# Kernel optimization log

Hardware: AMD Instinct MI355X
Metric: run time of the kernel (lower is better)

Reference implementation:

```python
import jax, jax.numpy as jnp
import numpy as np

NEUMANN_TERMS = 6  # matches neumann_terms=6 in init_kwargs


def cayley_apply(W, x, terms):
    """Apply Cayley-parameterized unitary U = (I - A)^{-1}(I + A), A = skew(W),
    with the inverse approximated by a truncated Neumann series:
    (I - A)^{-1} z ~= sum_{k=0}^{terms-1} A^k z.  x: [N, d] row vectors."""
    A = 0.5 * (W - W.T)            # skew-symmetric [d, d]
    z = x + x @ A.T                # (I + A) x
    acc = z
    s = z
    for _ in range(terms - 1):     # small fixed loop over Neumann terms
        s = s @ A.T                # A^k z
        acc = acc + s
    return acc


def quantum_activation(h, theta):
    """Parametric quantum rotation: rotate each adjacent feature pair by theta.
    Norm-preserving (unitary) nonlinearity in place of ReLU/GELU."""
    a = h[..., 0::2]
    b = h[..., 1::2]
    c = jnp.cos(theta)
    s = jnp.sin(theta)
    ra = a * c - b * s
    rb = a * s + b * c
    return jnp.stack([ra, rb], axis=-1).reshape(h.shape)


def setup_inputs() -> dict:
    key = jax.random.key(0)
    k1, k2, k3 = jax.random.split(key, 3)
    num_tokens, d_model = 16384, 2048
    x = jax.random.normal(k1, (num_tokens, d_model), dtype=jnp.float32)
    # Orthogonal(gain=0.1)-like init: small-norm weights keep the Neumann series convergent
    u1 = 0.1 * jax.random.normal(k2, (d_model, d_model), dtype=jnp.float32) / jnp.sqrt(d_model)
    u1 = u1 * jnp.sqrt(d_model) * 0.0 + 0.1 * jax.random.orthogonal(k2, d_model, dtype=jnp.float32)
    u2 = 0.1 * jax.random.orthogonal(k3, d_model, dtype=jnp.float32)
    theta = jnp.asarray(0.7854, dtype=jnp.float32)  # pi/4 initializer
    return {"x": x, "u1": u1, "u2": u2, "theta": theta}


def reference(x, u1, u2, theta):
    h = cayley_apply(u1, x, NEUMANN_TERMS)
    h = quantum_activation(h, theta)
    out = cayley_apply(u2, h, NEUMANN_TERMS)
    return out
```

## Files before the change

kernel.cpp:

```cpp
#include <hip/hip_runtime.h>
#include <hip/hip_bf16.h>

#define ND 2048

using bf16 = __hip_bfloat16;
using short8 = __attribute__((ext_vector_type(8))) short;
using floatx4 = __attribute__((ext_vector_type(4))) float;

__device__ __forceinline__ void gl2lds16(const short* g, short* l) {
    __builtin_amdgcn_global_load_lds(
        (const __attribute__((address_space(1))) unsigned int*)g,
        (__attribute__((address_space(3))) unsigned int*)l,
        16, 0, 0);
}

__device__ __forceinline__ int xcd_swz(int b, int g) {
    if ((g & 7) == 0) b = (b & 7) * (g >> 3) + (b >> 3);
    return b;
}


__global__ void build_skew2(const float* __restrict__ uA, bf16* __restrict__ MA,
                            const float* __restrict__ uB, bf16* __restrict__ MB) {
    __shared__ float t[32][33];
    const int nb = (ND / 32) * (ND / 32);
    int b = blockIdx.x;
    const float* u = uA;
    bf16* M = MA;
    if (b >= nb) { b -= nb; u = uB; M = MB; }
    const int bx = b & (ND / 32 - 1);
    const int by = b / (ND / 32);
    const int tx = threadIdx.x & 31;
    const int ty = threadIdx.x >> 5;
#pragma unroll
    for (int rr = 0; rr < 4; ++rr) {
        const int r = ty * 4 + rr;
        t[tx][r] = u[(size_t)(bx * 32 + r) * ND + by * 32 + tx];
    }
    __syncthreads();
#pragma unroll
    for (int rr = 0; rr < 4; ++rr) {
        const int r = ty * 4 + rr;
        const size_t idx = (size_t)(by * 32 + r) * ND + bx * 32 + tx;
        M[idx] = __float2bfloat16(0.5f * (t[r][tx] - u[idx]));
    }
}

__global__ void build_hoffs(const bf16* M2, const bf16* Q2, bf16* H2, bf16* HT2,
                            const bf16* M1, const bf16* Q1, bf16* H1) {
    const size_t nper = (size_t)ND * ND / 8;
    size_t g = (size_t)blockIdx.x * 256 + threadIdx.x;
    const bool second = (g >= nper);
    if (second) g -= nper;
    const size_t i8 = g * 8;
    const short8 mv = *(const short8*)((const short*)(second ? M1 : M2) + i8);
    const short8 qv = *(const short8*)((const short*)(second ? Q1 : Q2) + i8);
    short8 h, ht;
#pragma unroll
    for (int j = 0; j < 8; ++j) {
        const float m = __bfloat162float(__builtin_bit_cast(bf16, (short)mv[j]));
        const float q = __bfloat162float(__builtin_bit_cast(bf16, (short)qv[j]));
        h[j]  = __builtin_bit_cast(short, __float2bfloat16(2.f * m + q));
        ht[j] = __builtin_bit_cast(short, __float2bfloat16(q - 2.f * m));
    }
    if (second) {
        *(short8*)((short*)H1 + i8) = h;
    } else {
        *(short8*)((short*)H2 + i8) = h;
        *(short8*)((short*)HT2 + i8) = ht;
    }
}

__global__ void build_hoff(const bf16* M, const bf16* Msq, bf16* Hoff, bf16* HoffT) {
    const size_t idx = (size_t)blockIdx.x * 256 + threadIdx.x;
    const float m = __bfloat162float(M[idx]);
    const float q = __bfloat162float(Msq[idx]);
    Hoff[idx] = __float2bfloat16(2.f * m + q);
    HoffT[idx] = __float2bfloat16(q - 2.f * m);
}

__global__ void convert_f32_bf16(const float* __restrict__ x, bf16* __restrict__ y) {
    const size_t base = ((size_t)blockIdx.x * 256 + threadIdx.x) * 8;
    const float4 f0 = *(const float4*)(x + base);
    const float4 f1 = *(const float4*)(x + base + 4);
    short8 pk;
    pk[0] = __builtin_bit_cast(short, __float2bfloat16(f0.x));
    pk[1] = __builtin_bit_cast(short, __float2bfloat16(f0.y));
    pk[2] = __builtin_bit_cast(short, __float2bfloat16(f0.z));
    pk[3] = __builtin_bit_cast(short, __float2bfloat16(f0.w));
    pk[4] = __builtin_bit_cast(short, __float2bfloat16(f1.x));
    pk[5] = __builtin_bit_cast(short, __float2bfloat16(f1.y));
    pk[6] = __builtin_bit_cast(short, __float2bfloat16(f1.z));
    pk[7] = __builtin_bit_cast(short, __float2bfloat16(f1.w));
    *(short8*)((short*)y + base) = pk;
}

enum { EPI_PLAIN = 0, EPI_NEG = 1, EPI_ADD1 = 2, EPI_P = 3, EPI_P_ROT = 4 };

template <int EPI, bool OF32>
__device__ __forceinline__ void gemm_core(
    short* aT, short* bT,
    const bf16* __restrict__ A, const bf16* __restrict__ Bt, void* __restrict__ Cp,
    const int Nc, const int K, const int bx, const int by,
    const bf16* __restrict__ add1, const bf16* __restrict__ add2,
    const float* __restrict__ thetaP)
{
    const int tid = threadIdx.x;
    const int lane = tid & 63;
    const int quad = lane >> 4;
    const int l15 = lane & 15;
    const int wv = tid >> 6;
    const int wr = (wv >> 1) << 6;
    const int wc = (wv & 1) << 6;

    const short* Ag = (const short*)A + (size_t)(by << 7) * K;
    const short* Bg = (const short*)Bt + (size_t)(bx << 7) * K;

    floatx4 acc[4][4];
#pragma unroll
    for (int i = 0; i < 4; ++i)
#pragma unroll
        for (int j = 0; j < 4; ++j)
            acc[i][j] = (floatx4){0.f, 0.f, 0.f, 0.f};

    for (int k0 = 0; k0 < K; k0 += 32) {
#pragma unroll
        for (int c = 0; c < 2; ++c) {
            const int ch = (c << 8) + (wv << 6) + lane;
            const int row = ch >> 2;
            const int kp = (ch & 3) << 3;
            const int ldsBase = ((c << 8) + (wv << 6)) << 3;
            gl2lds16(Ag + (size_t)row * K + k0 + kp, aT + ldsBase);
            gl2lds16(Bg + (size_t)row * K + k0 + kp, bT + ldsBase);
        }
        __syncthreads();
        short8 af[4], bfr[4];
#pragma unroll
        for (int mi = 0; mi < 4; ++mi)
            af[mi] = *(const short8*)(aT + ((wr + (mi << 4) + l15) << 5) + (quad << 3));
#pragma unroll
        for (int ni = 0; ni < 4; ++ni)
            bfr[ni] = *(const short8*)(bT + ((wc + (ni << 4) + l15) << 5) + (quad << 3));
#pragma unroll
        for (int mi = 0; mi < 4; ++mi)
#pragma unroll
            for (int ni = 0; ni < 4; ++ni)
                acc[mi][ni] = __builtin_amdgcn_mfma_f32_16x16x32_bf16(af[mi], bfr[ni], acc[mi][ni], 0, 0, 0);
        __syncthreads();
    }

    float ct = 0.f, st = 0.f;
    if (EPI == EPI_P_ROT) {
        const float th = *thetaP;
        ct = cosf(th);
        st = sinf(th);
    }

#pragma unroll
    for (int mi = 0; mi < 4; ++mi) {
#pragma unroll
        for (int ni = 0; ni < 4; ++ni) {
#pragma unroll
            for (int r = 0; r < 4; ++r) {
                const int row = (by << 7) + wr + (mi << 4) + (quad << 2) + r;
                const int col = (bx << 7) + wc + (ni << 4) + l15;
                const size_t idx = (size_t)row * Nc + col;
                float v = acc[mi][ni][r];
                if (EPI == EPI_NEG) v = -v;
                if (EPI == EPI_ADD1) v += __bfloat162float(add1[idx]);
                if (EPI == EPI_P)
                    v += (row == col ? 1.f : 0.f)
                       + __bfloat162float(add1[idx]) + __bfloat162float(add2[idx]);
                if (EPI == EPI_P_ROT) {
                    v += (row == col ? 1.f : 0.f)
                       + __bfloat162float(add1[idx]) + __bfloat162float(add2[idx]);
                    const float w = __shfl_xor(v, 1, 64);
                    v = (l15 & 1) ? (st * w + ct * v) : (ct * v - st * w);
                }
                if (OF32) ((float*)Cp)[idx] = v;
                else      ((bf16*)Cp)[idx] = __float2bfloat16(v);
            }
        }
    }
}

template <int EPI, bool OF32>
__launch_bounds__(256, 2) __global__
void gemm_one(const bf16* __restrict__ A, const bf16* __restrict__ Bt,
              void* __restrict__ Cp, const int Nc, const int K,
              const bf16* __restrict__ add1, const bf16* __restrict__ add2,
              const float* __restrict__ thetaP)
{
    __shared__ __attribute__((aligned(16))) short aT[128 * 32];
    __shared__ __attribute__((aligned(16))) short bT[128 * 32];
    const int nblk = Nc >> 7;
    const int b = xcd_swz(blockIdx.x, gridDim.x);
    gemm_core<EPI, OF32>(aT, bT, A, Bt, Cp, Nc, K, b % nblk, b / nblk,
                         add1, add2, thetaP);
}

template <int EPI0, int EPI1>
__launch_bounds__(256, 2) __global__
void gemm_dual(const bf16* A0, const bf16* B0, bf16* C0, const bf16* a10, const bf16* a20,
               const bf16* A1, const bf16* B1, bf16* C1, const bf16* a11, const bf16* a21,
               const float* thetaP)
{
    __shared__ __attribute__((aligned(16))) short aT[128 * 32];
    __shared__ __attribute__((aligned(16))) short bT[128 * 32];
    const int nblk = ND >> 7;
    const int nsub = nblk * nblk;
    int b = xcd_swz(blockIdx.x, gridDim.x);
    if (b < nsub) {
        gemm_core<EPI0, false>(aT, bT, A0, B0, (void*)C0, ND, ND, b % nblk, b / nblk, a10, a20, thetaP);
    } else {
        b -= nsub;
        gemm_core<EPI1, false>(aT, bT, A1, B1, (void*)C1, ND, ND, b % nblk, b / nblk, a11, a21, thetaP);
    }
}


__device__ __forceinline__ void stage512(short* ldsT, const short* gT, const int K,
                                         const int kb, const int c0,
                                         const int wv, const int lane) {
    const int ch = c0 + (wv << 6) + lane;
    const int rw = ch >> 3;
    const int cs = (ch & 7) ^ (rw & 7);
    gl2lds16(gT + (size_t)rw * K + kb + (cs << 3),
             ldsT + ((c0 + (wv << 6)) << 3));
}

__device__ __forceinline__ void phase_mid() {
    __builtin_amdgcn_sched_barrier(0);
    __builtin_amdgcn_s_barrier();
    asm volatile("s_waitcnt lgkmcnt(0)" ::: "memory");
    __builtin_amdgcn_sched_barrier(0);
    __builtin_amdgcn_s_setprio(1);
}
__device__ __forceinline__ void phase_end() {
    __builtin_amdgcn_s_setprio(0);
    __builtin_amdgcn_sched_barrier(0);
    __builtin_amdgcn_s_barrier();
}

#define MFMA_BF16 __builtin_amdgcn_mfma_f32_16x16x32_bf16

__device__ __forceinline__ void tile256(
    short* Ac, short* Bc, short* An,
    const short* Ag, const short* Bg, const int K, const int nt, const int t,
    const int wv, const int lane, const int aBase, const int bBase,
    const int cOff0, const int cOff1, floatx4 (&acc)[8][4])
{
    short8 af[4][2], bb[4][2];
    const int kb1 = (t + 1) << 6;
    const int kb2 = (t + 2) << 6;

#pragma unroll
    for (int ml = 0; ml < 4; ++ml) {
        af[ml][0] = *(const short8*)(Ac + aBase + (ml << 10) + cOff0);
        af[ml][1] = *(const short8*)(Ac + aBase + (ml << 10) + cOff1);
    }
#pragma unroll
    for (int ni = 0; ni < 2; ++ni) {
        bb[ni][0] = *(const short8*)(Bc + bBase + (ni << 10) + cOff0);
        bb[ni][1] = *(const short8*)(Bc + bBase + (ni << 10) + cOff1);
    }
    if (t + 1 < nt) { stage512(An, Ag, K, kb1, 512, wv, lane); stage512(An, Ag, K, kb1, 1536, wv, lane); }
    __builtin_amdgcn_sched_barrier(0);
    asm volatile("s_waitcnt lgkmcnt(8)" ::: "memory");
    phase_mid();
#pragma unroll
    for (int ml = 0; ml < 4; ++ml)
#pragma unroll
        for (int ni = 0; ni < 2; ++ni) {
            acc[ml][ni] = MFMA_BF16(af[ml][0], bb[ni][0], acc[ml][ni], 0, 0, 0);
            acc[ml][ni] = MFMA_BF16(af[ml][1], bb[ni][1], acc[ml][ni], 0, 0, 0);
        }
    phase_end();

#pragma unroll
    for (int ni = 2; ni < 4; ++ni) {
        bb[ni][0] = *(const short8*)(Bc + bBase + (ni << 10) + cOff0);
        bb[ni][1] = *(const short8*)(Bc + bBase + (ni << 10) + cOff1);
    }
    if (t + 2 < nt) { stage512(Ac, Ag, K, kb2, 0, wv, lane); stage512(Ac, Ag, K, kb2, 1024, wv, lane); }
    phase_mid();
#pragma unroll
    for (int ml = 0; ml < 4; ++ml)
#pragma unroll
        for (int ni = 2; ni < 4; ++ni) {
            acc[ml][ni] = MFMA_BF16(af[ml][0], bb[ni][0], acc[ml][ni], 0, 0, 0);
            acc[ml][ni] = MFMA_BF16(af[ml][1], bb[ni][1], acc[ml][ni], 0, 0, 0);
        }
    phase_end();

#pragma unroll
    for (int ml = 0; ml < 4; ++ml) {
        af[ml][0] = *(const short8*)(Ac + aBase + 4096 + (ml << 10) + cOff0);
        af[ml][1] = *(const short8*)(Ac + aBase + 4096 + (ml << 10) + cOff1);
    }
    if (t + 2 < nt) { stage512(Bc, Bg, K, kb2, 0, wv, lane); stage512(Bc, Bg, K, kb2, 512, wv, lane); }
    phase_mid();
#pragma unroll
    for (int ml = 0; ml < 4; ++ml)
#pragma unroll
        for (int ni = 0; ni < 2; ++ni) {
            acc[4 + ml][ni] = MFMA_BF16(af[ml][0], bb[ni][0], acc[4 + ml][ni], 0, 0, 0);
            acc[4 + ml][ni] = MFMA_BF16(af[ml][1], bb[ni][1], acc[4 + ml][ni], 0, 0, 0);
        }
    phase_end();

    if (t + 2 < nt) { stage512(Bc, Bg, K, kb2, 1024, wv, lane); stage512(Bc, Bg, K, kb2, 1536, wv, lane); }
    __builtin_amdgcn_sched_barrier(0);
    if (t < nt - 2) asm volatile("s_waitcnt vmcnt(6)" ::: "memory");
    else            asm volatile("s_waitcnt vmcnt(0)" ::: "memory");
    __builtin_amdgcn_s_barrier();
    __builtin_amdgcn_sched_barrier(0);
    __builtin_amdgcn_s_setprio(1);
#pragma unroll
    for (int ml = 0; ml < 4; ++ml)
#pragma unroll
        for (int ni = 2; ni < 4; ++ni) {
            acc[4 + ml][ni] = MFMA_BF16(af[ml][0], bb[ni][0], acc[4 + ml][ni], 0, 0, 0);
            acc[4 + ml][ni] = MFMA_BF16(af[ml][1], bb[ni][1], acc[4 + ml][ni], 0, 0, 0);
        }
    phase_end();
}

__launch_bounds__(512, 2) __global__
void gemm_big256(const bf16* __restrict__ A, const bf16* __restrict__ Bt,
                 float* __restrict__ C, const int Nc, const int K)
{
    __shared__ __attribute__((aligned(16))) short smem[65536];
    short* A0s = smem;
    short* A1s = smem + 16384;
    short* B0s = smem + 32768;
    short* B1s = smem + 49152;

    const int nblkx = Nc >> 8;
    const int b = xcd_swz(blockIdx.x, gridDim.x);
    const int bx = b % nblkx;
    const int by = b / nblkx;
    const int tid = threadIdx.x;
    const int lane = tid & 63;
    const int q = lane >> 4;
    const int l15 = lane & 15;
    const int wv = tid >> 6;
    const int wm = wv >> 2;
    const int wn = wv & 3;

    const short* Ag = (const short*)A + (size_t)(by << 8) * K;
    const short* Bg = (const short*)Bt + (size_t)(bx << 8) * K;

    const int swz = l15 & 7;
    const int aBase = ((wm << 7) + l15) << 6;
    const int bBase = ((wn << 6) + l15) << 6;
    const int cOff0 = (q ^ swz) << 3;
    const int cOff1 = ((q + 4) ^ swz) << 3;

    floatx4 acc[8][4];
#pragma unroll
    for (int i = 0; i < 8; ++i)
#pragma unroll
        for (int j = 0; j < 4; ++j)
            acc[i][j] = (floatx4){0.f, 0.f, 0.f, 0.f};

    const int nt = K >> 6;

    stage512(A0s, Ag, K, 0, 0,    wv, lane);
    stage512(A0s, Ag, K, 0, 512,  wv, lane);
    stage512(A0s, Ag, K, 0, 1024, wv, lane);
    stage512(A0s, Ag, K, 0, 1536, wv, lane);
    stage512(B0s, Bg, K, 0, 0,    wv, lane);
    stage512(B0s, Bg, K, 0, 512,  wv, lane);
    stage512(B0s, Bg, K, 0, 1024, wv, lane);
    stage512(B0s, Bg, K, 0, 1536, wv, lane);
    stage512(A1s, Ag, K, 64, 0,    wv, lane);
    stage512(A1s, Ag, K, 64, 1024, wv, lane);
    stage512(B1s, Bg, K, 64, 0,    wv, lane);
    stage512(B1s, Bg, K, 64, 512,  wv, lane);
    stage512(B1s, Bg, K, 64, 1024, wv, lane);
    stage512(B1s, Bg, K, 64, 1536, wv, lane);
    __builtin_amdgcn_sched_barrier(0);
    asm volatile("s_waitcnt vmcnt(6)" ::: "memory");
    __builtin_amdgcn_s_barrier();

    for (int t = 0; t < nt; t += 2) {
        tile256(A0s, B0s, A1s, Ag, Bg, K, nt, t,     wv, lane, aBase, bBase, cOff0, cOff1, acc);
        tile256(A1s, B1s, A0s, Ag, Bg, K, nt, t + 1, wv, lane, aBase, bBase, cOff0, cOff1, acc);
    }

#pragma unroll
    for (int mi = 0; mi < 8; ++mi)
#pragma unroll
        for (int ni = 0; ni < 4; ++ni)
#pragma unroll
            for (int r = 0; r < 4; ++r) {
                const int row = (by << 8) + (wm << 7) + (mi << 4) + (q << 2) + r;
                const int col = (bx << 8) + (wn << 6) + (ni << 4) + l15;
                C[(size_t)row * Nc + col] = acc[mi][ni][r];
            }
}

template <int EPI, bool AF32, bool OF32>
__launch_bounds__(256, 2) __global__
void gemm_bt(const void* __restrict__ Ap, const bf16* __restrict__ Bt,
             void* __restrict__ Cp, const int Nc, const int K,
             const bf16* __restrict__ add1, const bf16* __restrict__ add2,
             const float* __restrict__ thetaP)
{
    __shared__ __attribute__((aligned(16))) short aT[128 * 32];
    __shared__ __attribute__((aligned(16))) short bT[128 * 32];

    const int nblk = Nc >> 7;
    const int bx = blockIdx.x % nblk;
    const int by = blockIdx.x / nblk;
    const int tid = threadIdx.x;
    const int lane = tid & 63;
    const int quad = lane >> 4;
    const int l15 = lane & 15;
    const int wv = tid >> 6;
    const int wr = (wv >> 1) << 6;
    const int wc = (wv & 1) << 6;

    const short* Ag = (const short*)Ap + (size_t)(by << 7) * K;
    const float* Agf = (const float*)Ap + (size_t)(by << 7) * K;
    const short* Bg = (const short*)Bt + (size_t)(bx << 7) * K;

    floatx4 acc[4][4];
#pragma unroll
    for (int i = 0; i < 4; ++i)
#pragma unroll
        for (int j = 0; j < 4; ++j)
            acc[i][j] = (floatx4){0.f, 0.f, 0.f, 0.f};

    for (int k0 = 0; k0 < K; k0 += 32) {
#pragma unroll
        for (int c = 0; c < 2; ++c) {
            const int ch = tid + (c << 8);
            const int row = ch >> 2;
            const int kp = (ch & 3) << 3;
            if (AF32) {
                const float4 f0 = *(const float4*)(Agf + (size_t)row * K + k0 + kp);
                const float4 f1 = *(const float4*)(Agf + (size_t)row * K + k0 + kp + 4);
                short8 pk;
                pk[0] = __builtin_bit_cast(short, __float2bfloat16(f0.x));
                pk[1] = __builtin_bit_cast(short, __float2bfloat16(f0.y));
                pk[2] = __builtin_bit_cast(short, __float2bfloat16(f0.z));
                pk[3] = __builtin_bit_cast(short, __float2bfloat16(f0.w));
                pk[4] = __builtin_bit_cast(short, __float2bfloat16(f1.x));
                pk[5] = __builtin_bit_cast(short, __float2bfloat16(f1.y));
                pk[6] = __builtin_bit_cast(short, __float2bfloat16(f1.z));
                pk[7] = __builtin_bit_cast(short, __float2bfloat16(f1.w));
                *(short8*)(aT + (row << 5) + kp) = pk;
            } else {
                *(int4*)(aT + (row << 5) + kp) = *(const int4*)(Ag + (size_t)row * K + k0 + kp);
            }
            *(int4*)(bT + (row << 5) + kp) = *(const int4*)(Bg + (size_t)row * K + k0 + kp);
        }
        __syncthreads();
        short8 af[4], bfr[4];
#pragma unroll
        for (int mi = 0; mi < 4; ++mi)
            af[mi] = *(const short8*)(aT + ((wr + (mi << 4) + l15) << 5) + (quad << 3));
#pragma unroll
        for (int ni = 0; ni < 4; ++ni)
            bfr[ni] = *(const short8*)(bT + ((wc + (ni << 4) + l15) << 5) + (quad << 3));
#pragma unroll
        for (int mi = 0; mi < 4; ++mi)
#pragma unroll
            for (int ni = 0; ni < 4; ++ni)
                acc[mi][ni] = __builtin_amdgcn_mfma_f32_16x16x32_bf16(af[mi], bfr[ni], acc[mi][ni], 0, 0, 0);
        __syncthreads();
    }

    float ct = 0.f, st = 0.f;
    if (EPI == EPI_P_ROT) {
        const float th = *thetaP;
        ct = cosf(th);
        st = sinf(th);
    }

#pragma unroll
    for (int mi = 0; mi < 4; ++mi) {
#pragma unroll
        for (int ni = 0; ni < 4; ++ni) {
#pragma unroll
            for (int r = 0; r < 4; ++r) {
                const int row = (by << 7) + wr + (mi << 4) + (quad << 2) + r;
                const int col = (bx << 7) + wc + (ni << 4) + l15;
                const size_t idx = (size_t)row * Nc + col;
                float v = acc[mi][ni][r];
                if (EPI == EPI_NEG) v = -v;
                if (EPI == EPI_ADD1) v += __bfloat162float(add1[idx]);
                if (EPI == EPI_P || EPI == EPI_P_ROT)
                    v += (row == col ? 1.f : 0.f)
                       + __bfloat162float(add1[idx]) + __bfloat162float(add2[idx]);
                if (EPI == EPI_P_ROT) {
                    const float w = __shfl_xor(v, 1, 64);
                    v = (l15 & 1) ? (st * w + ct * v) : (ct * v - st * w);
                }
                if (OF32) ((float*)Cp)[idx] = v;
                else      ((bf16*)Cp)[idx] = __float2bfloat16(v);
            }
        }
    }
}


extern "C" void kernel_launch(void* const* d_in, const int* in_sizes, int n_in,
                              void* d_out, int out_size, void* d_ws, size_t ws_size,
                              hipStream_t stream)
{
    const float* x = (const float*)d_in[0];
    const float* u1 = (const float*)d_in[1];
    const float* u2 = (const float*)d_in[2];
    const float* th = (const float*)d_in[3];
    float* out = (float*)d_out;
    const int tokens = in_sizes[0] / ND;

    const size_t MAT = (size_t)ND * ND;
    const size_t XBE = (size_t)tokens * ND;

    const dim3 blk(256);
    const int gSkew = (ND / 32) * (ND / 32);
    const int gElem = (int)(MAT / 256);
    const int gSm = (ND / 128) * (ND / 128);
    const int gBig = (tokens / 128) * (ND / 128);

    if (ws_size >= (6 * MAT + XBE) * sizeof(bf16)) {
        bf16* base = (bf16*)d_ws;
        bf16* b0 = base;
        bf16* b1 = base + MAT;
        bf16* b2 = base + 2 * MAT;
        bf16* b3 = base + 3 * MAT;
        bf16* b4 = base + 4 * MAT;
        bf16* b5 = base + 5 * MAT;
        bf16* xb = base + 6 * MAT;

        convert_f32_bf16<<<(int)(XBE / 2048), blk, 0, stream>>>(x, xb);
        build_skew2<<<2 * gSkew, blk, 0, stream>>>(u2, b0, u1, b1);
        gemm_dual<EPI_NEG, EPI_NEG><<<2 * gSm, blk, 0, stream>>>(
            b0, b0, b2, nullptr, nullptr,  b1, b1, b3, nullptr, nullptr, nullptr);
        gemm_dual<EPI_ADD1, EPI_ADD1><<<2 * gSm, blk, 0, stream>>>(
            b2, b2, b4, b2, nullptr,  b3, b3, b5, b3, nullptr, nullptr);
        build_hoffs<<<(int)(2 * MAT / 2048), blk, 0, stream>>>(b0, b2, b2, b0, b1, b3, b3);
        gemm_dual<EPI_P, EPI_P_ROT><<<2 * gSm, blk, 0, stream>>>(
            b4, b2, b0, b4, b0,  b3, b5, b1, b5, b3, th);
        gemm_one<EPI_PLAIN, false><<<gSm, blk, 0, stream>>>(b0, b1, b2, ND, ND, nullptr, nullptr, nullptr);
        if ((tokens & 255) == 0) {
            const int gBig256 = (tokens >> 8) * (ND >> 8);
            gemm_big256<<<gBig256, dim3(512), 0, stream>>>(xb, b2, out, ND, ND);
        } else {
            gemm_one<EPI_PLAIN, true><<<gBig, blk, 0, stream>>>(xb, b2, out, ND, ND, nullptr, nullptr, nullptr);
        }
    } else {
        bf16* A = (bf16*)d_ws;
        bf16* B = A + MAT;
        bf16* Cb = B + MAT;
        bf16* D = Cb + MAT;
        bf16* E = D + MAT;

        build_skew2<<<gSkew, blk, 0, stream>>>(u2, A, u2, A);
        gemm_bt<EPI_NEG, false, false><<<gSm, blk, 0, stream>>>(A, A, B, ND, ND, nullptr, nullptr, nullptr);
        gemm_bt<EPI_ADD1, false, false><<<gSm, blk, 0, stream>>>(B, B, Cb, ND, ND, B, nullptr, nullptr);
        build_hoff<<<gElem, blk, 0, stream>>>(A, B, D, E);
        gemm_bt<EPI_P, false, false><<<gSm, blk, 0, stream>>>(Cb, D, A, ND, ND, Cb, E, nullptr);

        build_skew2<<<gSkew, blk, 0, stream>>>(u1, B, u1, B);
        gemm_bt<EPI_NEG, false, false><<<gSm, blk, 0, stream>>>(B, B, Cb, ND, ND, nullptr, nullptr, nullptr);
        gemm_bt<EPI_ADD1, false, false><<<gSm, blk, 0, stream>>>(Cb, Cb, D, ND, ND, Cb, nullptr, nullptr);
        build_hoff<<<gElem, blk, 0, stream>>>(B, Cb, E, B);
        gemm_bt<EPI_P_ROT, false, false><<<gSm, blk, 0, stream>>>(E, D, Cb, ND, ND, D, E, th);

        gemm_bt<EPI_PLAIN, false, false><<<gSm, blk, 0, stream>>>(A, Cb, D, ND, ND, nullptr, nullptr, nullptr);
        gemm_bt<EPI_PLAIN, true, true><<<gBig, blk, 0, stream>>>(x, D, out, ND, ND, nullptr, nullptr, nullptr);
    }
}
```

Baseline: 563.9 us.

## Split-K the 2048x2048 weight-composition GEMMs with fp32 partials and reduce kernels

Replaces the dual 128-tile GEMMs that build the composite weight matrices with a split-K 256-tile GEMM (gemm_sk), which writes fp32 partial sums into the output buffer used as scratch. Separate elementwise reduce kernels then sum the partials and apply the epilogues (negate, add, identity, theta rotation). The aim is to fill the GPU better, since a 2048x2048 GEMM with 256 tiles gives only 64 blocks, and to reuse the faster 256-tile pipeline. In exchange it adds extra fp32 traffic and more kernel launches, and the scratch reuse depends on the output buffer being large enough.

Measured after the change: 593.6 us. 5.3% more time.

```diff
diff --git a/kernel.cpp b/kernel.cpp
--- a/kernel.cpp
+++ b/kernel.cpp
@@ -93,6 +93,122 @@
     pk[6] = __builtin_bit_cast(short, __float2bfloat16(f1.z));
     pk[7] = __builtin_bit_cast(short, __float2bfloat16(f1.w));
     *(short8*)((short*)y + base) = pk;
+}
+
+__device__ __forceinline__ void loadS8(const float* p, float (&v)[8]) {
+    const float4 a = *(const float4*)p;
+    const float4 b = *(const float4*)(p + 4);
+    v[0] = a.x; v[1] = a.y; v[2] = a.z; v[3] = a.w;
+    v[4] = b.x; v[5] = b.y; v[6] = b.z; v[7] = b.w;
+}
+#define BF(x)   __bfloat162float(__builtin_bit_cast(bf16, (short)(x)))
+#define TOBF(x) __builtin_bit_cast(short, __float2bfloat16(x))
+
+__global__ void red_msq_hoff(const float* __restrict__ S,
+                             bf16* M2io ,
+                             bf16* M1io ,
+                             bf16* Msq2o , bf16* Msq1o ,
+                             bf16* Hoff2o ) {
+    const size_t MATE = (size_t)ND * ND;
+    const size_t nper = MATE / 8;
+    size_t g = (size_t)blockIdx.x * 256 + threadIdx.x;
+    const bool c1 = (g >= nper);
+    if (c1) g -= nper;
+    const size_t i8 = g * 8;
+    const float* s0 = S + (c1 ? 2 * MATE : 0) + i8;
+    float p0[8], p1[8];
+    loadS8(s0, p0); loadS8(s0 + MATE, p1);
+    const short8 mv = *(const short8*)((const short*)(c1 ? M1io : M2io) + i8);
+    short8 msq, hf, ht;
+#pragma unroll
+    for (int j = 0; j < 8; ++j) {
+        const short qb = TOBF(-(p0[j] + p1[j]));
+        msq[j] = qb;
+        const float q = BF(qb);
+        const float m = BF(mv[j]);
+        hf[j] = TOBF(2.f * m + q);
+        ht[j] = TOBF(q - 2.f * m);
+    }
+    if (c1) {
+        *(short8*)((short*)Msq1o + i8) = msq;
+        *(short8*)((short*)M1io + i8) = hf;
+    } else {
+        *(short8*)((short*)Msq2o + i8) = msq;
+        *(short8*)((short*)Hoff2o + i8) = hf;
+        *(short8*)((short*)M2io + i8) = ht;
+    }
+}
+
+__global__ void red_goff(const float* __restrict__ S, bf16* g2io , bf16* g1io ) {
+    const size_t MATE = (size_t)ND * ND;
+    const size_t nper = MATE / 8;
+    size_t g = (size_t)blockIdx.x * 256 + threadIdx.x;
+    const bool c1 = (g >= nper);
+    if (c1) g -= nper;
+    const size_t i8 = g * 8;
+    const float* s0 = S + (c1 ? 2 * MATE : 0) + i8;
+    float p0[8], p1[8];
+    loadS8(s0, p0); loadS8(s0 + MATE, p1);
+    const short8 av = *(const short8*)((const short*)(c1 ? g1io : g2io) + i8);
+    short8 o;
+#pragma unroll
+    for (int j = 0; j < 8; ++j)
+        o[j] = TOBF((p0[j] + p1[j]) + BF(av[j]));
+    *(short8*)((short*)(c1 ? g1io : g2io) + i8) = o;
+}
+
+__global__ void red_p(const float* __restrict__ S,
+                      bf16* p2t , const bf16* goff2 ,
+                      bf16* p1r , const bf16* goff1 ,
+                      const float* __restrict__ thetaP) {
+    const size_t MATE = (size_t)ND * ND;
+    const size_t nper = MATE / 8;
+    size_t g = (size_t)blockIdx.x * 256 + threadIdx.x;
+    const bool c1 = (g >= nper);
+    if (c1) g -= nper;
+    const size_t i8 = g * 8;
+    const float* s0 = S + (c1 ? 2 * MATE : 0) + i8;
+    float p0[8], p1[8];
+    loadS8(s0, p0); loadS8(s0 + MATE, p1);
+    const short8 a1v = *(const short8*)((const short*)(c1 ? goff1 : goff2) + i8);
+    const short8 a2v = *(const short8*)((const short*)(c1 ? p1r : p2t) + i8);
+    float v[8];
+#pragma unroll
+    for (int j = 0; j < 8; ++j) {
+        const size_t e = i8 + j;
+        const float diag = ((e >> 11) == (e & (ND - 1))) ? 1.f : 0.f;
+        v[j] = p0[j] + p1[j];
+        v[j] += diag + BF(a1v[j]) + BF(a2v[j]);
+    }
+    short8 o;
+    if (c1) {
+        const float th = *thetaP;
+        const float ct = cosf(th), st = sinf(th);
+#pragma unroll
+        for (int j = 0; j < 8; j += 2) {
+            const float a = v[j], b = v[j + 1];
+            o[j]     = TOBF(ct * a - st * b);
+            o[j + 1] = TOBF(st * a + ct * b);
+        }
+        *(short8*)((short*)p1r + i8) = o;
+    } else {
+#pragma unroll
+        for (int j = 0; j < 8; ++j) o[j] = TOBF(v[j]);
+        *(short8*)((short*)p2t + i8) = o;
+    }
+}
+
+__global__ void red_qt(const float* __restrict__ S, bf16* __restrict__ q) {
+    const size_t MATE = (size_t)ND * ND;
+    const size_t i8 = ((size_t)blockIdx.x * 256 + threadIdx.x) * 8;
+    float p0[8], p1[8], p2[8], p3[8];
+    loadS8(S + i8, p0); loadS8(S + MATE + i8, p1);
+    loadS8(S + 2 * MATE + i8, p2); loadS8(S + 3 * MATE + i8, p3);
+    short8 o;
+#pragma unroll
+    for (int j = 0; j < 8; ++j)
+        o[j] = TOBF(((p0[j] + p1[j]) + p2[j]) + p3[j]);
+    *(short8*)((short*)q + i8) = o;
 }
 
 enum { EPI_PLAIN = 0, EPI_NEG = 1, EPI_ADD1 = 2, EPI_P = 3, EPI_P_ROT = 4 };
@@ -247,12 +363,13 @@
 __device__ __forceinline__ void tile256(
     short* Ac, short* Bc, short* An,
     const short* Ag, const short* Bg, const int K, const int nt, const int t,
+    const int kOff,
     const int wv, const int lane, const int aBase, const int bBase,
     const int cOff0, const int cOff1, floatx4 (&acc)[8][4])
 {
     short8 af[4][2], bb[4][2];
-    const int kb1 = (t + 1) << 6;
-    const int kb2 = (t + 2) << 6;
+    const int kb1 = kOff + ((t + 1) << 6);
+    const int kb2 = kOff + ((t + 2) << 6);
 
 #pragma unroll
     for (int ml = 0; ml < 4; ++ml) {
@@ -385,8 +502,8 @@
     __builtin_amdgcn_s_barrier();
 
     for (int t = 0; t < nt; t += 2) {
-        tile256(A0s, B0s, A1s, Ag, Bg, K, nt, t,     wv, lane, aBase, bBase, cOff0, cOff1, acc);
-        tile256(A1s, B1s, A0s, Ag, Bg, K, nt, t + 1, wv, lane, aBase, bBase, cOff0, cOff1, acc);
+        tile256(A0s, B0s, A1s, Ag, Bg, K, nt, t,     0, wv, lane, aBase, bBase, cOff0, cOff1, acc);
+        tile256(A1s, B1s, A0s, Ag, Bg, K, nt, t + 1, 0, wv, lane, aBase, bBase, cOff0, cOff1, acc);
     }
 
 #pragma unroll
@@ -398,6 +515,88 @@
                 const int row = (by << 8) + (wm << 7) + (mi << 4) + (q << 2) + r;
                 const int col = (bx << 8) + (wn << 6) + (ni << 4) + l15;
                 C[(size_t)row * Nc + col] = acc[mi][ni][r];
+            }
+}
+
+template <int NT>
+__launch_bounds__(512, 2) __global__
+void gemm_sk(const bf16* __restrict__ A0, const bf16* __restrict__ B0,
+             const bf16* __restrict__ A1, const bf16* __restrict__ B1,
+             float* __restrict__ S)
+{
+    __shared__ __attribute__((aligned(16))) short smem[65536];
+    short* A0s = smem;
+    short* A1s = smem + 16384;
+    short* B0s = smem + 32768;
+    short* B1s = smem + 49152;
+
+    const int b = xcd_swz(blockIdx.x, gridDim.x);
+    const int sub = b >> 6;
+    const int t6 = b & 63;
+    const int bx = t6 & 7;
+    const int by = t6 >> 3;
+    const bf16* A; const bf16* Bt; int kOff;
+    if (NT == 16) { A = (sub & 2) ? A1 : A0; Bt = (sub & 2) ? B1 : B0; kOff = (sub & 1) << 10; }
+    else          { A = A0; Bt = B0; kOff = sub << 9; }
+    float* C = S + (size_t)sub * ((size_t)ND * ND);
+    const int K = ND;
+
+    const int tid = threadIdx.x;
+    const int lane = tid & 63;
+    const int q = lane >> 4;
+    const int l15 = lane & 15;
+    const int wv = tid >> 6;
+    const int wm = wv >> 2;
+    const int wn = wv & 3;
+
+    const short* Ag = (const short*)A + (size_t)(by << 8) * K;
+    const short* Bg = (const short*)Bt + (size_t)(bx << 8) * K;
+
+    const int swz = l15 & 7;
+    const int aBase = ((wm << 7) + l15) << 6;
+    const int bBase = ((wn << 6) + l15) << 6;
+    const int cOff0 = (q ^ swz) << 3;
+    const int cOff1 = ((q + 4) ^ swz) << 3;
+
+    floatx4 acc[8][4];
+#pragma unroll
+    for (int i = 0; i < 8; ++i)
+#pragma unroll
+        for (int j = 0; j < 4; ++j)
+            acc[i][j] = (floatx4){0.f, 0.f, 0.f, 0.f};
+
+    stage512(A0s, Ag, K, kOff, 0,    wv, lane);
+    stage512(A0s, Ag, K, kOff, 512,  wv, lane);
+    stage512(A0s, Ag, K, kOff, 1024, wv, lane);
+    stage512(A0s, Ag, K, kOff, 1536, wv, lane);
+    stage512(B0s, Bg, K, kOff, 0,    wv, lane);
+    stage512(B0s, Bg, K, kOff, 512,  wv, lane);
+    stage512(B0s, Bg, K, kOff, 1024, wv, lane);
+    stage512(B0s, Bg, K, kOff, 1536, wv, lane);
+    stage512(A1s, Ag, K, kOff + 64, 0,    wv, lane);
+    stage512(A1s, Ag, K, kOff + 64, 1024, wv, lane);
+    stage512(B1s, Bg, K, kOff + 64, 0,    wv, lane);
+    stage512(B1s, Bg, K, kOff + 64, 512,  wv, lane);
+    stage512(B1s, Bg, K, kOff + 64, 1024, wv, lane);
+    stage512(B1s, Bg, K, kOff + 64, 1536, wv, lane);
+    __builtin_amdgcn_sched_barrier(0);
+    asm volatile("s_waitcnt vmcnt(6)" ::: "memory");
+    __builtin_amdgcn_s_barrier();
+
+    for (int t = 0; t < NT; t += 2) {
+        tile256(A0s, B0s, A1s, Ag, Bg, K, NT, t,     kOff, wv, lane, aBase, bBase, cOff0, cOff1, acc);
+        tile256(A1s, B1s, A0s, Ag, Bg, K, NT, t + 1, kOff, wv, lane, aBase, bBase, cOff0, cOff1, acc);
+    }
+
+#pragma unroll
+    for (int mi = 0; mi < 8; ++mi)
+#pragma unroll
+        for (int ni = 0; ni < 4; ++ni)
+#pragma unroll
+            for (int r = 0; r < 4; ++r) {
+                const int row = (by << 8) + (wm << 7) + (mi << 4) + (q << 2) + r;
+                const int col = (bx << 8) + (wn << 6) + (ni << 4) + l15;
+                C[(size_t)row * ND + col] = acc[mi][ni][r];
             }
 }
 
@@ -534,23 +733,34 @@
         bf16* b2 = base + 2 * MAT;
         bf16* b3 = base + 3 * MAT;
         bf16* b4 = base + 4 * MAT;
-        bf16* b5 = base + 5 * MAT;
         bf16* xb = base + 6 * MAT;
 
         convert_f32_bf16<<<(int)(XBE / 2048), blk, 0, stream>>>(x, xb);
         build_skew2<<<2 * gSkew, blk, 0, stream>>>(u2, b0, u1, b1);
-        gemm_dual<EPI_NEG, EPI_NEG><<<2 * gSm, blk, 0, stream>>>(
-            b0, b0, b2, nullptr, nullptr,  b1, b1, b3, nullptr, nullptr, nullptr);
-        gemm_dual<EPI_ADD1, EPI_ADD1><<<2 * gSm, blk, 0, stream>>>(
-            b2, b2, b4, b2, nullptr,  b3, b3, b5, b3, nullptr, nullptr);
-        build_hoffs<<<(int)(2 * MAT / 2048), blk, 0, stream>>>(b0, b2, b2, b0, b1, b3, b3);
-        gemm_dual<EPI_P, EPI_P_ROT><<<2 * gSm, blk, 0, stream>>>(
-            b4, b2, b0, b4, b0,  b3, b5, b1, b5, b3, th);
-        gemm_one<EPI_PLAIN, false><<<gSm, blk, 0, stream>>>(b0, b1, b2, ND, ND, nullptr, nullptr, nullptr);
-        if ((tokens & 255) == 0) {
+
+        if ((tokens & 255) == 0 && (size_t)out_size >= 8 * MAT * sizeof(float)) {
+            float* S = out;
+            const int gRed = (int)(2 * MAT / 2048);
+            gemm_sk<16><<<256, dim3(512), 0, stream>>>(b0, b0, b1, b1, S);
+            red_msq_hoff<<<gRed, blk, 0, stream>>>(S, b0, b1, b2, b3, b4);
+            gemm_sk<16><<<256, dim3(512), 0, stream>>>(b2, b2, b3, b3, S);
+            red_goff<<<gRed, blk, 0, stream>>>(S, b2, b3);
+            gemm_sk<16><<<256, dim3(512), 0, stream>>>(b2, b4, b1, b3, S);
+            red_p<<<gRed, blk, 0, stream>>>(S, b0, b2, b1, b3, th);
+            gemm_sk<8><<<256, dim3(512), 0, stream>>>(b0, b1, nullptr, nullptr, S);
+            red_qt<<<(int)(MAT / 2048), blk, 0, stream>>>(S, b2);
             const int gBig256 = (tokens >> 8) * (ND >> 8);
             gemm_big256<<<gBig256, dim3(512), 0, stream>>>(xb, b2, out, ND, ND);
         } else {
+            bf16* b5 = base + 5 * MAT;
+            gemm_dual<EPI_NEG, EPI_NEG><<<2 * gSm, blk, 0, stream>>>(
+                b0, b0, b2, nullptr, nullptr,  b1, b1, b3, nullptr, nullptr, nullptr);
+            gemm_dual<EPI_ADD1, EPI_ADD1><<<2 * gSm, blk, 0, stream>>>(
+                b2, b2, b4, b2, nullptr,  b3, b3, b5, b3, nullptr, nullptr);
+            build_hoffs<<<(int)(2 * MAT / 2048), blk, 0, stream>>>(b0, b2, b2, b0, b1, b3, b3);
+            gemm_dual<EPI_P, EPI_P_ROT><<<2 * gSm, blk, 0, stream>>>(
+                b4, b2, b0, b4, b0,  b3, b5, b1, b5, b3, th);
+            gemm_one<EPI_PLAIN, false><<<gSm, blk, 0, stream>>>(b0, b1, b2, ND, ND, nullptr, nullptr, nullptr);
             gemm_one<EPI_PLAIN, true><<<gBig, blk, 0, stream>>>(xb, b2, out, ND, ND, nullptr, nullptr, nullptr);
         }
     } else {
```
